# Kernel optimization log

Measured on AMD Instinct MI355X. Metric: run time of the kernel, lower is better.

## Reference

```python
import jax, jax.numpy as jnp
import numpy as np

B, L, E, H, FF = 2, 2048, 1024, 16, 4096
DH = E // H
EPS = 1e-5
# NOTE: source has attn_scale = 1 / dh**(-0.5) == sqrt(dh) (multiplies, not divides)
ATTN_SCALE = float(DH) ** 0.5


def _layernorm(x, w, b):
    mu = jnp.mean(x, axis=-1, keepdims=True)
    var = jnp.mean((x - mu) ** 2, axis=-1, keepdims=True)
    return (x - mu) * jax.lax.rsqrt(var + EPS) * w + b


def setup_inputs() -> dict:
    key = jax.random.key(0)
    ks = jax.random.split(key, 8)
    s = 0.02
    return {
        "x": jax.random.normal(ks[0], (B, L, E), jnp.float32),
        "ln1_w": jnp.ones((E,), jnp.float32),
        "ln1_b": jnp.zeros((E,), jnp.float32),
        "wq": jax.random.normal(ks[1], (E, E), jnp.float32) * s,
        "bq": jnp.zeros((E,), jnp.float32),
        "wk": jax.random.normal(ks[2], (E, E), jnp.float32) * s,
        "bk": jnp.zeros((E,), jnp.float32),
        "wv": jax.random.normal(ks[3], (E, E), jnp.float32) * s,
        "bv": jnp.zeros((E,), jnp.float32),
        "wo": jax.random.normal(ks[4], (E, E), jnp.float32) * s,
        "bo": jnp.zeros((E,), jnp.float32),
        "ln2_w": jnp.ones((E,), jnp.float32),
        "ln2_b": jnp.zeros((E,), jnp.float32),
        "wu": jax.random.normal(ks[5], (E, FF), jnp.float32) * s,
        "bu": jnp.zeros((FF,), jnp.float32),
        "wd": jax.random.normal(ks[6], (FF, E), jnp.float32) * s,
        "bd": jnp.zeros((E,), jnp.float32),
    }


def reference(x, ln1_w, ln1_b, wq, bq, wk, bk, wv, bv, wo, bo,
              ln2_w, ln2_b, wu, bu, wd, bd):
    # --- attention block (pre-LN, manual softmax attention) ---
    xn = _layernorm(x, ln1_w, ln1_b)                       # [B,L,E]
    q = (xn @ wq + bq).reshape(B, L, H, DH)
    k = (xn @ wk + bk).reshape(B, L, H, DH)
    v = (xn @ wv + bv).reshape(B, L, H, DH)
    score = jnp.einsum("blhd,bmhd->bhlm", q, k) * ATTN_SCALE  # [B,H,L,L]
    attn = jax.nn.softmax(score, axis=-1)
    ctx = jnp.einsum("bhlm,bmhd->blhd", attn, v).reshape(B, L, E)
    hidden = x + (ctx @ wo + bo)
    # --- FFN block (pre-LN, GELU) ---
    hn = _layernorm(hidden, ln2_w, ln2_b)
    up = jax.nn.gelu(hn @ wu + bu, approximate=False)      # [B,L,F]
    down = up @ wd + bd
    return hidden + down
```

## Files before the change

kernel.cpp:

```cpp
#include <hip/hip_runtime.h>
#include <stdint.h>


typedef __attribute__((ext_vector_type(8))) short short8;
typedef __attribute__((ext_vector_type(4))) float floatx4;
typedef __attribute__((ext_vector_type(16))) float floatx16;

extern "C" __device__ float __ocml_native_exp2_f32(float);
#define EXP2(x) __ocml_native_exp2_f32(x)

#define MFMA_BF16(a, b, c) __builtin_amdgcn_mfma_f32_16x16x32_bf16((a), (b), (c), 0, 0, 0)
#define MFMA32(a, b, c) __builtin_amdgcn_mfma_f32_32x32x16_bf16((a), (b), (c), 0, 0, 0)

__device__ __forceinline__ unsigned short f2bf(float f) {
  union { float f; unsigned int u; } v; v.f = f;
  unsigned int r = v.u + 0x7FFFu + ((v.u >> 16) & 1u);
  return (unsigned short)(r >> 16);
}

__device__ __forceinline__ unsigned int f2u(float f) {
  union { float f; unsigned int u; } v; v.f = f; return v.u;
}

__device__ __forceinline__ short8 pack4(unsigned a, unsigned b, unsigned c, unsigned d) {
  union { unsigned u[4]; short8 s; } v;
  v.u[0] = a; v.u[1] = b; v.u[2] = c; v.u[3] = d;
  return v.s;
}

__device__ __forceinline__ void gl_lds16(const unsigned short* g, unsigned short* l) {
  __builtin_amdgcn_global_load_lds(
      (const __attribute__((address_space(1))) unsigned int*)g,
      (__attribute__((address_space(3))) unsigned int*)l, 16, 0, 0);
}

template <int MODE, int BN>
__global__ __launch_bounds__(256)
void gemm_bt(const unsigned short* __restrict__ A,
             const unsigned short* __restrict__ Bt,
             const float* __restrict__ bias,
             void* __restrict__ outp,
             const float* __restrict__ res,
             int K,
             void* __restrict__ out2, void* __restrict__ out3,
             const float* __restrict__ bias2, const float* __restrict__ bias3) {
  constexpr int BM = 128, BK = 64;
  constexpr int MI = (BN == 128) ? 4 : 2;
  constexpr int NI = 4;
  __shared__ __align__(16) unsigned short As[BM * BK];
  __shared__ __align__(16) unsigned short Bs[BN * BK];
  const int tid = threadIdx.x;
  const int wave = tid >> 6, lane = tid & 63, l16 = lane & 15, quad = lane >> 4;
  const int m0 = blockIdx.y * BM, n0 = blockIdx.x * BN;
  const int wm = (BN == 128) ? (wave >> 1) * 64 : wave * 32;
  const int wn = (BN == 128) ? (wave & 1) * 64 : 0;
  const int sw = l16 & 7;
  const int sl0 = (quad ^ sw) << 3;
  const int sl1 = sl0 ^ 32;

  floatx4 acc[MI][NI] = {};

  for (int k0 = 0; k0 < K; k0 += BK) {
    __syncthreads();
#pragma unroll
    for (int c = 0; c < (BM * BK) / 2048; ++c) {
      const int e = (c * 256 + tid) * 8;
      const int row = e >> 6, c8 = (e >> 3) & 7;
      gl_lds16(A + (size_t)(m0 + row) * K + k0 + ((c8 ^ (row & 7)) << 3), &As[e]);
    }
#pragma unroll
    for (int c = 0; c < (BN * BK) / 2048; ++c) {
      const int e = (c * 256 + tid) * 8;
      const int row = e >> 6, c8 = (e >> 3) & 7;
      gl_lds16(Bt + (size_t)(n0 + row) * K + k0 + ((c8 ^ (row & 7)) << 3), &Bs[e]);
    }
    __syncthreads();

    short8 af0[MI], af1[MI], bf0[NI], bf1[NI];
#pragma unroll
    for (int i = 0; i < MI; ++i) {
      af0[i] = *(const short8*)&As[(wm + i * 16 + l16) * BK + sl0];
      af1[i] = *(const short8*)&As[(wm + i * 16 + l16) * BK + sl1];
    }
#pragma unroll
    for (int i = 0; i < NI; ++i) {
      bf0[i] = *(const short8*)&Bs[(wn + i * 16 + l16) * BK + sl0];
      bf1[i] = *(const short8*)&Bs[(wn + i * 16 + l16) * BK + sl1];
    }
#pragma unroll
    for (int mi = 0; mi < MI; ++mi)
#pragma unroll
      for (int ni = 0; ni < NI; ++ni) {
        acc[mi][ni] = MFMA_BF16(af0[mi], bf0[ni], acc[mi][ni]);
        acc[mi][ni] = MFMA_BF16(af1[mi], bf1[ni], acc[mi][ni]);
      }
  }

  const int seg = (MODE == 0) ? (n0 >> 10) : 0;
  const float* bptr = bias;
  if constexpr (MODE == 0) bptr = (seg == 0) ? bias : (seg == 1 ? bias2 : bias3);

  float bcol[NI];
#pragma unroll
  for (int ni = 0; ni < NI; ++ni) {
    const int n = n0 + wn + ni * 16 + l16;
    bcol[ni] = bptr[(MODE == 0) ? (n & 1023) : n];
  }

#pragma unroll
  for (int mi = 0; mi < MI; ++mi) {
#pragma unroll
    for (int r = 0; r < 4; ++r) {
      const int m = m0 + wm + mi * 16 + quad * 4 + r;
#pragma unroll
      for (int ni = 0; ni < NI; ++ni) {
        const int n = n0 + wn + ni * 16 + l16;
        const float c = acc[mi][ni][r] + bcol[ni];
        if constexpr (MODE == 0) {
          const int b_ = m >> 11, l = m & 2047, hd = n & 1023;
          const size_t idx =
              ((size_t)((b_ * 16 + (hd >> 6)) * 2048 + l)) * 64 + (hd & 63);
          if (seg == 0)       ((unsigned short*)outp)[idx] = f2bf(c * 11.5415603270f);
          else if (seg == 1)  ((unsigned short*)out2)[idx] = f2bf(c);
          else                ((unsigned short*)out3)[idx] = f2bf(c);
        } else if constexpr (MODE == 1) {
          ((float*)outp)[(size_t)m * 1024 + n] = res[(size_t)m * 1024 + n] + c;
        } else if constexpr (MODE == 2) {
          const float g = 0.5f * c * (1.0f + erff(c * 0.70710678118654752f));
          ((unsigned short*)outp)[(size_t)m * 4096 + n] = f2bf(g);
        } else {
          ((float*)outp)[(size_t)m * 1024 + n] = res[(size_t)m * 1024 + n] + c;
        }
      }
    }
  }
}

__global__ __launch_bounds__(256)
void layernorm_kernel(const float* __restrict__ x, const float* __restrict__ w,
                      const float* __restrict__ b, unsigned short* __restrict__ out) {
  const int row = blockIdx.x, tid = threadIdx.x;
  const int wave = tid >> 6, lane = tid & 63;
  const float4 v = ((const float4*)(x + (size_t)row * 1024))[tid];
  float s = v.x + v.y + v.z + v.w;
  float s2 = v.x * v.x + v.y * v.y + v.z * v.z + v.w * v.w;
#pragma unroll
  for (int off = 32; off > 0; off >>= 1) {
    s += __shfl_down(s, off);
    s2 += __shfl_down(s2, off);
  }
  __shared__ float red[8];
  if (lane == 0) { red[wave] = s; red[4 + wave] = s2; }
  __syncthreads();
  const float ts = red[0] + red[1] + red[2] + red[3];
  const float ts2 = red[4] + red[5] + red[6] + red[7];
  const float mu = ts * (1.0f / 1024.0f);
  const float var = ts2 * (1.0f / 1024.0f) - mu * mu;
  const float rs = rsqrtf(var + 1e-5f);
  const float4 wv = ((const float4*)w)[tid];
  const float4 bv = ((const float4*)b)[tid];
  ushort4 o;
  o.x = f2bf((v.x - mu) * rs * wv.x + bv.x);
  o.y = f2bf((v.y - mu) * rs * wv.y + bv.y);
  o.z = f2bf((v.z - mu) * rs * wv.z + bv.z);
  o.w = f2bf((v.w - mu) * rs * wv.w + bv.w);
  ((ushort4*)(out + (size_t)row * 1024))[tid] = o;
}

__global__ __launch_bounds__(256)
void transpose_cast4(const float* __restrict__ s0, const float* __restrict__ s1,
                     const float* __restrict__ s2, const float* __restrict__ s3,
                     unsigned short* __restrict__ dst) {
  __shared__ float tile[32][33];
  const int z = blockIdx.z;
  const float* in = (z == 0) ? s0 : (z == 1) ? s1 : (z == 2) ? s2 : s3;
  unsigned short* out = dst + (size_t)z * 1024 * 1024;
  const int tx = threadIdx.x, ty = threadIdx.y;
  const int c0 = blockIdx.x * 32, r0 = blockIdx.y * 32;
#pragma unroll
  for (int i = 0; i < 4; ++i)
    tile[ty + 8 * i][tx] = in[(size_t)(r0 + ty + 8 * i) * 1024 + c0 + tx];
  __syncthreads();
#pragma unroll
  for (int i = 0; i < 4; ++i)
    out[(size_t)(c0 + ty + 8 * i) * 1024 + r0 + tx] = f2bf(tile[tx][ty + 8 * i]);
}

__global__ __launch_bounds__(256)
void transpose_cast(const float* __restrict__ in, unsigned short* __restrict__ out,
                    int R, int C) {
  __shared__ float tile[32][33];
  const int tx = threadIdx.x, ty = threadIdx.y;
  const int c0 = blockIdx.x * 32, r0 = blockIdx.y * 32;
#pragma unroll
  for (int i = 0; i < 4; ++i)
    tile[ty + 8 * i][tx] = in[(size_t)(r0 + ty + 8 * i) * C + c0 + tx];
  __syncthreads();
#pragma unroll
  for (int i = 0; i < 4; ++i)
    out[(size_t)(c0 + ty + 8 * i) * R + r0 + tx] = f2bf(tile[tx][ty + 8 * i]);
}

__global__ __launch_bounds__(256)
void transpose_bf16(const unsigned short* __restrict__ in,
                    unsigned short* __restrict__ out, int R, int C) {
  __shared__ unsigned short tile[32][33];
  const size_t hoff = (size_t)blockIdx.z * R * C;
  in += hoff; out += hoff;
  const int tx = threadIdx.x, ty = threadIdx.y;
  const int c0 = blockIdx.x * 32, r0 = blockIdx.y * 32;
#pragma unroll
  for (int i = 0; i < 4; ++i)
    tile[ty + 8 * i][tx] = in[(size_t)(r0 + ty + 8 * i) * C + c0 + tx];
  __syncthreads();
  const int txp = (tx & ~12) | ((tx & 4) << 1) | ((tx & 8) >> 1);
#pragma unroll
  for (int i = 0; i < 4; ++i)
    out[(size_t)(c0 + ty + 8 * i) * R + r0 + txp] = tile[tx][ty + 8 * i];
}

__global__ __launch_bounds__(256, 4)
void flash_attn(const unsigned short* __restrict__ q,
                const unsigned short* __restrict__ k,
                const unsigned short* __restrict__ v,
                unsigned short* __restrict__ ctx) {
  __shared__ __align__(16) unsigned short Ks[2][64 * 64];
  __shared__ __align__(16) unsigned short Vs[2][64 * 64];
  const int bh = blockIdx.y, qt = blockIdx.x;
  const int tid = threadIdx.x, wave = tid >> 6, lane = tid & 63;
  const int qw = wave & 1, kw = wave >> 1;
  const int lo = lane & 31, hi = lane >> 5, sw7 = lo & 7;
  const unsigned short* kb = k + (size_t)bh * 2048 * 64;
  const unsigned short* vb = v + (size_t)bh * 64 * 2048;

  const int qrow = qt * 64 + qw * 32 + lo;
  const unsigned short* qp = q + ((size_t)bh * 2048 + qrow) * 64;
  short8 qf[4];
#pragma unroll
  for (int kq = 0; kq < 4; ++kq) qf[kq] = *(const short8*)(qp + kq * 16 + hi * 8);

  int co[4];
#pragma unroll
  for (int j = 0; j < 4; ++j) co[j] = ((j * 2 + hi) ^ sw7) << 3;

  floatx16 O0 = {}, O1 = {};
  float m_run = -1e30f, l_run = 0.f;

  auto stage = [&](int t, int bufi) {
    const int kv0 = t * 64;
#pragma unroll
    for (int c = 0; c < 2; ++c) {
      const int e = (c * 256 + tid) * 8;
      const int r = e >> 6, ch = (e >> 3) & 7;
      const int sc = ((ch ^ (r & 7)) << 3);
      gl_lds16(kb + (size_t)(kv0 + r) * 64 + sc, &Ks[bufi][e]);
      gl_lds16(vb + (size_t)r * 2048 + kv0 + sc, &Vs[bufi][e]);
    }
  };
  stage(0, 0);

  for (int t = 0; t < 32; ++t) {
    __syncthreads();
    const int bufi = t & 1;
    if (t + 1 < 32) stage(t + 1, bufi ^ 1);

    const unsigned short* Kb = &Ks[bufi][0];
    const unsigned short* Vb = &Vs[bufi][0];

    floatx16 st = {};
    __builtin_amdgcn_s_setprio(1);
#pragma unroll
    for (int kq = 0; kq < 4; ++kq) {
      const short8 kf = *(const short8*)&Kb[(kw * 32 + lo) * 64 + co[kq]];
      st = MFMA32(kf, qf[kq], st);
    }
    __builtin_amdgcn_s_setprio(0);

    float mp[4];
#pragma unroll
    for (int r = 0; r < 4; ++r)
      mp[r] = fmaxf(fmaxf(st[r], st[r + 4]), fmaxf(st[r + 8], st[r + 12]));
    float mx = fmaxf(fmaxf(mp[0], mp[1]), fmaxf(mp[2], mp[3]));
    mx = fmaxf(mx, __shfl_xor(mx, 32));
    if (!__all(mx - m_run <= 8.0f)) {
      const float m_new = fmaxf(m_run, mx);
      const float alpha = EXP2(m_run - m_new);
      m_run = m_new;
      l_run *= alpha;
#pragma unroll
      for (int r = 0; r < 16; ++r) { O0[r] *= alpha; O1[r] *= alpha; }
    }
#pragma unroll
    for (int r = 0; r < 16; ++r) st[r] = EXP2(st[r] - m_run);
    float sp[4];
#pragma unroll
    for (int r = 0; r < 4; ++r)
      sp[r] = (st[r] + st[r + 4]) + (st[r + 8] + st[r + 12]);
    float rsum = (sp[0] + sp[1]) + (sp[2] + sp[3]);
    rsum += __shfl_xor(rsum, 32);
    l_run += rsum;

    unsigned pw[8];
#pragma unroll
    for (int i = 0; i < 8; ++i)
      pw[i] = __builtin_amdgcn_perm(f2u(st[2 * i + 1]), f2u(st[2 * i]), 0x07060302u);
    const short8 pf0 = pack4(pw[0], pw[1], pw[2], pw[3]);
    const short8 pf1 = pack4(pw[4], pw[5], pw[6], pw[7]);

    __builtin_amdgcn_s_setprio(1);
    {
      const short8 vf00 = *(const short8*)&Vb[lo * 64 + co[2 * kw]];
      const short8 vf01 = *(const short8*)&Vb[(32 + lo) * 64 + co[2 * kw]];
      O0 = MFMA32(vf00, pf0, O0);
      O1 = MFMA32(vf01, pf0, O1);
      const short8 vf10 = *(const short8*)&Vb[lo * 64 + co[2 * kw + 1]];
      const short8 vf11 = *(const short8*)&Vb[(32 + lo) * 64 + co[2 * kw + 1]];
      O0 = MFMA32(vf10, pf1, O0);
      O1 = MFMA32(vf11, pf1, O1);
    }
    __builtin_amdgcn_s_setprio(0);
  }

  __syncthreads();
  float* Os = (float*)&Ks[0][0];
  float* Ml = (float*)&Vs[0][0];
  if (kw == 1) {
    float* o = Os + (size_t)(qw * 64 + lane) * 32;
#pragma unroll
    for (int r = 0; r < 16; ++r) {
      o[(r + lane) & 31] = O0[r];
      o[(16 + r + lane) & 31] = O1[r];
    }
    Ml[qw * 64 + lane] = m_run;
    Ml[128 + qw * 64 + lane] = l_run;
  }
  __syncthreads();
  if (kw == 0) {
    const float m2 = Ml[qw * 64 + lane];
    const float l2 = Ml[128 + qw * 64 + lane];
    const float m = fmaxf(m_run, m2);
    const float a1 = EXP2(m_run - m), a2 = EXP2(m2 - m);
    const float linv = 1.0f / (l_run * a1 + l2 * a2);
    const float* o = Os + (size_t)(qw * 64 + lane) * 32;
    float f0[16], f1[16];
#pragma unroll
    for (int r = 0; r < 16; ++r) {
      f0[r] = (O0[r] * a1 + o[(r + lane) & 31] * a2) * linv;
      f1[r] = (O1[r] * a1 + o[(16 + r + lane) & 31] * a2) * linv;
    }
    const int b_ = bh >> 4, h_ = bh & 15;
    unsigned short* op = ctx + ((size_t)(b_ * 2048) + qrow) * 1024 + h_ * 64;
#pragma unroll
    for (int rq = 0; rq < 4; ++rq) {
      ushort4 a4, b4;
      a4.x = f2bf(f0[rq * 4 + 0]); a4.y = f2bf(f0[rq * 4 + 1]);
      a4.z = f2bf(f0[rq * 4 + 2]); a4.w = f2bf(f0[rq * 4 + 3]);
      *(ushort4*)(op + rq * 8 + hi * 4) = a4;
      b4.x = f2bf(f1[rq * 4 + 0]); b4.y = f2bf(f1[rq * 4 + 1]);
      b4.z = f2bf(f1[rq * 4 + 2]); b4.w = f2bf(f1[rq * 4 + 3]);
      *(ushort4*)(op + 32 + rq * 8 + hi * 4) = b4;
    }
  }
}

extern "C" void kernel_launch(void* const* d_in, const int* in_sizes, int n_in,
                              void* d_out, int out_size, void* d_ws, size_t ws_size,
                              hipStream_t stream) {
  const float* x     = (const float*)d_in[0];
  const float* ln1_w = (const float*)d_in[1];
  const float* ln1_b = (const float*)d_in[2];
  const float* wq    = (const float*)d_in[3];
  const float* bq    = (const float*)d_in[4];
  const float* wk    = (const float*)d_in[5];
  const float* bk    = (const float*)d_in[6];
  const float* wv    = (const float*)d_in[7];
  const float* bv    = (const float*)d_in[8];
  const float* wo    = (const float*)d_in[9];
  const float* bo    = (const float*)d_in[10];
  const float* ln2_w = (const float*)d_in[11];
  const float* ln2_b = (const float*)d_in[12];
  const float* wu    = (const float*)d_in[13];
  const float* bu    = (const float*)d_in[14];
  const float* wd    = (const float*)d_in[15];
  const float* bd    = (const float*)d_in[16];

  char* W = (char*)d_ws;
  const size_t MB = 1ull << 20;
  unsigned short* wqkvT = (unsigned short*)(W + 0 * MB);
  unsigned short* woT   = (unsigned short*)(W + 6 * MB);
  unsigned short* wuT   = (unsigned short*)(W + 8 * MB);
  unsigned short* wdT   = (unsigned short*)(W + 16 * MB);
  unsigned short* xn    = (unsigned short*)(W + 24 * MB);
  unsigned short* qb    = (unsigned short*)(W + 32 * MB);
  unsigned short* kb    = (unsigned short*)(W + 40 * MB);
  unsigned short* vb    = (unsigned short*)(W + 48 * MB);
  unsigned short* cx    = (unsigned short*)(W + 56 * MB);
  float*          hid   = (float*)(W + 64 * MB);
  unsigned short* up    = (unsigned short*)(W + 24 * MB);

  const dim3 tb(32, 8);
  transpose_cast4<<<dim3(32, 32, 4), tb, 0, stream>>>(wq, wk, wv, wo, wqkvT);
  transpose_cast<<<dim3(128, 32), tb, 0, stream>>>(wu, wuT, 1024, 4096);
  transpose_cast<<<dim3(32, 128), tb, 0, stream>>>(wd, wdT, 4096, 1024);

  layernorm_kernel<<<4096, 256, 0, stream>>>(x, ln1_w, ln1_b, xn);
  gemm_bt<0, 128><<<dim3(24, 32), 256, 0, stream>>>(
      xn, wqkvT, bq, qb, nullptr, 1024, kb, cx, bk, bv);
  transpose_bf16<<<dim3(2, 64, 32), tb, 0, stream>>>(cx, vb, 2048, 64);
  flash_attn<<<dim3(32, 32), 256, 0, stream>>>(qb, kb, vb, cx);
  gemm_bt<1, 64><<<dim3(16, 32), 256, 0, stream>>>(
      cx, woT, bo, hid, x, 1024, nullptr, nullptr, nullptr, nullptr);

  layernorm_kernel<<<4096, 256, 0, stream>>>(hid, ln2_w, ln2_b, cx);
  gemm_bt<2, 128><<<dim3(32, 32), 256, 0, stream>>>(
      cx, wuT, bu, up, nullptr, 1024, nullptr, nullptr, nullptr, nullptr);
  gemm_bt<3, 64><<<dim3(16, 32), 256, 0, stream>>>(
      up, wdT, bd, d_out, hid, 4096, nullptr, nullptr, nullptr, nullptr);
}
```

Measured before the change: 403.6 us.

## Add triple-buffered async-LDS GEMM for residual projections and swizzle attention block order

```diff
diff --git a/kernel.cpp b/kernel.cpp
--- a/kernel.cpp
+++ b/kernel.cpp
@@ -136,6 +136,100 @@
   }
 }
 
+__device__ __forceinline__ void stage_p3(const unsigned short* __restrict__ A,
+                                         const unsigned short* __restrict__ Bt,
+                                         int K, int m0, int n0, int k0, int tid,
+                                         unsigned short* Asb, unsigned short* Bsb) {
+#pragma unroll
+  for (int c = 0; c < 4; ++c) {
+    const int e = (c * 256 + tid) * 8;
+    const int row = e >> 6, c8 = (e >> 3) & 7;
+    gl_lds16(A + (size_t)(m0 + row) * K + k0 + ((c8 ^ (row & 7)) << 3), Asb + e);
+  }
+#pragma unroll
+  for (int c = 0; c < 2; ++c) {
+    const int e = (c * 256 + tid) * 8;
+    const int row = e >> 6, c8 = (e >> 3) & 7;
+    gl_lds16(Bt + (size_t)(n0 + row) * K + k0 + ((c8 ^ (row & 7)) << 3), Bsb + e);
+  }
+}
+
+__global__ __launch_bounds__(256)
+void gemm_bt_p3(const unsigned short* __restrict__ A,
+                const unsigned short* __restrict__ Bt,
+                const float* __restrict__ bias,
+                float* __restrict__ outp,
+                const float* __restrict__ res,
+                int K) {
+  constexpr int BM = 128, BN = 64, BK = 64, MI = 2, NI = 4;
+  __shared__ __align__(16) unsigned short As[3][BM * BK];
+  __shared__ __align__(16) unsigned short Bs[3][BN * BK];
+  const int tid = threadIdx.x;
+  const int wave = tid >> 6, lane = tid & 63, l16 = lane & 15, quad = lane >> 4;
+  const int m0 = blockIdx.y * BM, n0 = blockIdx.x * BN;
+  const int wm = wave * 32;
+  const int sw = l16 & 7;
+  const int sl0 = (quad ^ sw) << 3;
+  const int sl1 = sl0 ^ 32;
+
+  floatx4 acc[MI][NI] = {};
+
+  const int nt = K / BK;
+  stage_p3(A, Bt, K, m0, n0, 0 * BK, tid, As[0], Bs[0]);
+  stage_p3(A, Bt, K, m0, n0, 1 * BK, tid, As[1], Bs[1]);
+  stage_p3(A, Bt, K, m0, n0, 2 * BK, tid, As[2], Bs[2]);
+
+  for (int t = 0; t < nt; ++t) {
+    if (t < nt - 2)       asm volatile("s_waitcnt vmcnt(12)" ::: "memory");
+    else if (t == nt - 2) asm volatile("s_waitcnt vmcnt(6)" ::: "memory");
+    else                  asm volatile("s_waitcnt vmcnt(0)" ::: "memory");
+    __builtin_amdgcn_s_barrier();
+
+    const unsigned short* Ab = As[t % 3];
+    const unsigned short* Bb = Bs[t % 3];
+    short8 af0[MI], af1[MI], bf0[NI], bf1[NI];
+#pragma unroll
+    for (int i = 0; i < MI; ++i) {
+      af0[i] = *(const short8*)&Ab[(wm + i * 16 + l16) * BK + sl0];
+      af1[i] = *(const short8*)&Ab[(wm + i * 16 + l16) * BK + sl1];
+    }
+#pragma unroll
+    for (int i = 0; i < NI; ++i) {
+      bf0[i] = *(const short8*)&Bb[(i * 16 + l16) * BK + sl0];
+      bf1[i] = *(const short8*)&Bb[(i * 16 + l16) * BK + sl1];
+    }
+#pragma unroll
+    for (int mi = 0; mi < MI; ++mi)
+#pragma unroll
+      for (int ni = 0; ni < NI; ++ni) {
+        acc[mi][ni] = MFMA_BF16(af0[mi], bf0[ni], acc[mi][ni]);
+        acc[mi][ni] = MFMA_BF16(af1[mi], bf1[ni], acc[mi][ni]);
+      }
+
+    __builtin_amdgcn_s_barrier();
+    if (t + 3 < nt)
+      stage_p3(A, Bt, K, m0, n0, (t + 3) * BK, tid, As[t % 3], Bs[t % 3]);
+  }
+
+  float bcol[NI];
+#pragma unroll
+  for (int ni = 0; ni < NI; ++ni) bcol[ni] = bias[n0 + ni * 16 + l16];
+
+#pragma unroll
+  for (int mi = 0; mi < MI; ++mi) {
+#pragma unroll
+    for (int r = 0; r < 4; ++r) {
+      const int m = m0 + wm + mi * 16 + quad * 4 + r;
+#pragma unroll
+      for (int ni = 0; ni < NI; ++ni) {
+        const int n = n0 + ni * 16 + l16;
+        const float c = acc[mi][ni][r] + bcol[ni];
+        outp[(size_t)m * 1024 + n] = res[(size_t)m * 1024 + n] + c;
+      }
+    }
+  }
+}
+
 __global__ __launch_bounds__(256)
 void layernorm_kernel(const float* __restrict__ x, const float* __restrict__ w,
                       const float* __restrict__ b, unsigned short* __restrict__ out) {
@@ -226,7 +320,9 @@
                 unsigned short* __restrict__ ctx) {
   __shared__ __align__(16) unsigned short Ks[2][64 * 64];
   __shared__ __align__(16) unsigned short Vs[2][64 * 64];
-  const int bh = blockIdx.y, qt = blockIdx.x;
+  const int bid = blockIdx.x + (blockIdx.y << 5);
+  const int wg = (bid & 7) * 128 + (bid >> 3);
+  const int bh = wg >> 5, qt = wg & 31;
   const int tid = threadIdx.x, wave = tid >> 6, lane = tid & 63;
   const int qw = wave & 1, kw = wave >> 1;
   const int lo = lane & 31, hi = lane >> 5, sw7 = lo & 7;
@@ -408,12 +504,12 @@
       xn, wqkvT, bq, qb, nullptr, 1024, kb, cx, bk, bv);
   transpose_bf16<<<dim3(2, 64, 32), tb, 0, stream>>>(cx, vb, 2048, 64);
   flash_attn<<<dim3(32, 32), 256, 0, stream>>>(qb, kb, vb, cx);
-  gemm_bt<1, 64><<<dim3(16, 32), 256, 0, stream>>>(
-      cx, woT, bo, hid, x, 1024, nullptr, nullptr, nullptr, nullptr);
+  gemm_bt_p3<<<dim3(16, 32), 256, 0, stream>>>(
+      cx, woT, bo, hid, x, 1024);
 
   layernorm_kernel<<<4096, 256, 0, stream>>>(hid, ln2_w, ln2_b, cx);
   gemm_bt<2, 128><<<dim3(32, 32), 256, 0, stream>>>(
       cx, wuT, bu, up, nullptr, 1024, nullptr, nullptr, nullptr, nullptr);
-  gemm_bt<3, 64><<<dim3(16, 32), 256, 0, stream>>>(
-      up, wdT, bd, d_out, hid, 4096, nullptr, nullptr, nullptr, nullptr);
-}
+  gemm_bt_p3<<<dim3(16, 32), 256, 0, stream>>>(
+      up, wdT, bd, (float*)d_out, hid, 4096);
+}
```

New measurement: 384.4 us. 1.05x faster.
